# Performance work log

Measured on AMD Instinct MI355X. Metric: run time of the kernel, lower is better.

## Reference

```python
import jax, jax.numpy as jnp
import numpy as np

T, B, V, HID, L = 1024, 64, 256, 512, 2


def setup_inputs() -> dict:
    key = jax.random.key(0)
    ks = jax.random.split(key, 6)
    inputs = jax.random.normal(ks[0], (T, B, V), jnp.float32)
    H = jax.random.normal(ks[1], (L, B, HID), jnp.float32) * 0.1
    s1 = 1.0 / np.sqrt(V + HID)   # torch Linear default init bound
    W_net = jax.random.uniform(ks[2], (HID, V + HID), jnp.float32, -s1, s1)
    b_net = jax.random.uniform(ks[3], (HID,), jnp.float32, -s1, s1)
    s2 = 1.0 / np.sqrt(2 * HID)
    W_deep = jax.random.uniform(ks[4], (HID, 2 * HID), jnp.float32, -s2, s2)
    b_deep = jax.random.uniform(ks[5], (HID,), jnp.float32, -s2, s2)
    return {"inputs": inputs, "H": H, "W_net": W_net, "b_net": b_net,
            "W_deep": W_deep, "b_deep": b_deep}


def _rnn_scan(xs, h0, W, b):
    # xs: [T, B, Din], h0: [B, HID]; torch does tanh(cat(x, h) @ W.T + b)
    Din = xs.shape[-1]
    Wx, Wh = W[:, :Din], W[:, Din:]  # split cat-matmul into two GEMMs (same math)
    def step(h, x):
        h = jnp.tanh(x @ Wx.T + h @ Wh.T + b)
        return h, h
    last, states = jax.lax.scan(step, h0, xs)
    return states, last  # [T, B, HID], [B, HID]


def reference(inputs, H, W_net, b_net, W_deep, b_deep):
    all_states, last = _rnn_scan(inputs, H[0], W_net, b_net)
    last_states = [last]
    for l in range(1, H.shape[0]):  # deep layers: input dim = HID
        all_states, last = _rnn_scan(all_states, H[l], W_deep, b_deep)
        last_states.append(last)
    return all_states, jnp.stack(last_states)  # [T,B,HID], [L,B,HID]
```

## Files before the change

### kernel.cpp

```cpp
#include <hip/hip_runtime.h>
#include <hip/hip_fp16.h>
#include <cstdint>
#include <cstddef>

#define TT 1024
#define BB 64
#define VV 256
#define HH 512
static const size_t TBH = (size_t)TT * BB * HH;

#define AGENT __HIP_MEMORY_SCOPE_AGENT

typedef _Float16 half2v __attribute__((ext_vector_type(2)));
union U32H2 { unsigned u; half2v h; };

__device__ __forceinline__ unsigned pack_f16x2(float a, float b) {
    __half ha = __float2half_rn(a);
    __half hb = __float2half_rn(b);
    return (unsigned)__half_as_ushort(ha) | ((unsigned)__half_as_ushort(hb) << 16);
}

__device__ __forceinline__ float tanh_fast(float x) {
    float ax = fabsf(x);
    float e = __expf(-2.0f * ax);
    float r = (1.0f - e) * __builtin_amdgcn_rcpf(1.0f + e);
    return copysignf(r, x);
}

__device__ __forceinline__ float fdot2(unsigned w, unsigned h, float acc) {
    U32H2 uw; uw.u = w;
    U32H2 uh; uh.u = h;
#if __has_builtin(__builtin_amdgcn_fdot2)
    return __builtin_amdgcn_fdot2(uw.h, uh.h, acc, false);
#else
    return acc + (float)uw.h[0] * (float)uh.h[0] + (float)uw.h[1] * (float)uh.h[1];
#endif
}

__global__ void pack_weights(const float* __restrict__ Wnet,
                             const float* __restrict__ Wdeep,
                             unsigned* __restrict__ Wq0, unsigned* __restrict__ Wq1,
                             unsigned* __restrict__ Wp0, unsigned* __restrict__ Wp1) {
    int id = blockIdx.x * 256 + threadIdx.x;
    const int NQ  = HH * (HH / 2);
    const int NP0 = (VV / 2) * HH;
    const int NP1 = (HH / 2) * HH;
    if (id < NQ) {
        int i = id >> 8, jp = id & 255;
        const float* row = Wnet + (size_t)i * (VV + HH) + VV;
        Wq0[id] = pack_f16x2(row[2 * jp], row[2 * jp + 1]);
        return;
    }
    id -= NQ;
    if (id < NQ) {
        int i = id >> 8, jp = id & 255;
        const float* row = Wdeep + (size_t)i * (2 * HH) + HH;
        Wq1[id] = pack_f16x2(row[2 * jp], row[2 * jp + 1]);
        return;
    }
    id -= NQ;
    if (id < NP0) {
        int k2 = id >> 9, n = id & 511;
        const float* row = Wnet + (size_t)n * (VV + HH);
        Wp0[id] = pack_f16x2(row[2 * k2], row[2 * k2 + 1]);
        return;
    }
    id -= NP0;
    if (id < NP1) {
        int k2 = id >> 9, n = id & 511;
        const float* row = Wdeep + (size_t)n * (2 * HH);
        Wp1[id] = pack_f16x2(row[2 * k2], row[2 * k2 + 1]);
        return;
    }
}

__device__ __forceinline__ void dot8(float* acc, unsigned a, uint4 w0, uint4 w1) {
    acc[0] = fdot2(w0.x, a, acc[0]);
    acc[1] = fdot2(w0.y, a, acc[1]);
    acc[2] = fdot2(w0.z, a, acc[2]);
    acc[3] = fdot2(w0.w, a, acc[3]);
    acc[4] = fdot2(w1.x, a, acc[4]);
    acc[5] = fdot2(w1.y, a, acc[5]);
    acc[6] = fdot2(w1.z, a, acc[6]);
    acc[7] = fdot2(w1.w, a, acc[7]);
}

__launch_bounds__(1024)
__global__ void xproj_f16(const float* __restrict__ A,
                          const unsigned* __restrict__ Wp,
                          const float* __restrict__ bias,
                          float* __restrict__ C, int K) {
    extern __shared__ unsigned As2[];
    const int m0 = blockIdx.x * 32;
    const int t = threadIdx.x;
    const int K2 = K >> 1;

    const int nf4 = 8 * K;
    const float4* Ag = (const float4*)(A + (size_t)m0 * K);
    for (int idx = t; idx < nf4; idx += 1024) {
        float4 v = Ag[idx];
        As2[idx * 2]     = pack_f16x2(v.x, v.y);
        As2[idx * 2 + 1] = pack_f16x2(v.z, v.w);
    }
    __syncthreads();

    const int rg = t >> 6;
    const int n0 = (t & 63) * 8;

    float acc0[8] = {0, 0, 0, 0, 0, 0, 0, 0};
    float acc1[8] = {0, 0, 0, 0, 0, 0, 0, 0};

    const unsigned* a0p = As2 + (size_t)(rg * 2) * K2;
    const unsigned* a1p = a0p + K2;

#pragma unroll 4
    for (int k2 = 0; k2 < K2; k2 += 2) {
        unsigned a00 = a0p[k2], a01 = a0p[k2 + 1];
        unsigned a10 = a1p[k2], a11 = a1p[k2 + 1];
        const uint4 w00 = *(const uint4*)(Wp + (size_t)k2 * 512 + n0);
        const uint4 w01 = *(const uint4*)(Wp + (size_t)k2 * 512 + n0 + 4);
        const uint4 w10 = *(const uint4*)(Wp + (size_t)(k2 + 1) * 512 + n0);
        const uint4 w11 = *(const uint4*)(Wp + (size_t)(k2 + 1) * 512 + n0 + 4);
        dot8(acc0, a00, w00, w01);
        dot8(acc1, a10, w00, w01);
        dot8(acc0, a01, w10, w11);
        dot8(acc1, a11, w10, w11);
    }

    float bv[8];
#pragma unroll
    for (int c = 0; c < 8; ++c) bv[c] = bias[n0 + c];

    float* Crow0 = C + (size_t)(m0 + rg * 2) * 512 + n0;
    float* Crow1 = Crow0 + 512;
    *(float4*)(Crow0)     = make_float4(acc0[0] + bv[0], acc0[1] + bv[1], acc0[2] + bv[2], acc0[3] + bv[3]);
    *(float4*)(Crow0 + 4) = make_float4(acc0[4] + bv[4], acc0[5] + bv[5], acc0[6] + bv[6], acc0[7] + bv[7]);
    *(float4*)(Crow1)     = make_float4(acc1[0] + bv[0], acc1[1] + bv[1], acc1[2] + bv[2], acc1[3] + bv[3]);
    *(float4*)(Crow1 + 4) = make_float4(acc1[4] + bv[4], acc1[5] + bv[5], acc1[6] + bv[6], acc1[7] + bv[7]);
}

__launch_bounds__(512, 1)
__global__ void rnn_scan3(const unsigned* __restrict__ Wq,
                          const float* __restrict__ h0,
                          float* __restrict__ states,
                          float* __restrict__ last,
                          unsigned long long* __restrict__ X) {
    __shared__ float hsh[2][256];

    const int w = blockIdx.x;
    const int b = w & 63;
    const int s = w >> 6;
    const int r = threadIdx.x;
    const int lane = r & 63;
    const int owner = r >> 8;
    const bool is_owner = (owner == s);

    uint4 wreg[32];
    {
        const uint4* Wr = (const uint4*)(Wq + (size_t)r * 256 + s * 128);
#pragma unroll
        for (int q = 0; q < 32; ++q) wreg[q] = Wr[q];
    }

    unsigned hp[2];
    {
        const float2* h2 = (const float2*)(h0 + (size_t)b * HH);
#pragma unroll
        for (int rr = 0; rr < 2; ++rr) {
            float2 v = h2[s * 128 + rr * 64 + lane];
            hp[rr] = pack_f16x2(v.x, v.y);
        }
    }

    unsigned long long* slotA = X + ((((size_t)b * 2 + owner) * 2 + 0) << 8) + (r & 255);
    unsigned long long* slotB = slotA + 256;

    size_t base = (size_t)b * HH;
    const size_t tstride = (size_t)BB * HH;

    float pre_cur = 0.f;
    if (is_owner) pre_cur = states[base + r];

    float h = 0.f;
    for (int t = 0; t < TT; ++t) {
        float pre_nxt = 0.f;
        if (is_owner && t + 1 < TT) pre_nxt = states[base + tstride + r];

        float a0 = 0.f, a1 = 0.f, a2 = 0.f, a3 = 0.f;
#pragma unroll
        for (int q = 0; q < 32; ++q) {
            const uint4 wv = wreg[q];
            const int j = q * 4;
            unsigned s0 = (unsigned)__builtin_amdgcn_readlane((int)hp[(j + 0) >> 6], (j + 0) & 63);
            unsigned s1 = (unsigned)__builtin_amdgcn_readlane((int)hp[(j + 1) >> 6], (j + 1) & 63);
            unsigned s2 = (unsigned)__builtin_amdgcn_readlane((int)hp[(j + 2) >> 6], (j + 2) & 63);
            unsigned s3 = (unsigned)__builtin_amdgcn_readlane((int)hp[(j + 3) >> 6], (j + 3) & 63);
            a0 = fdot2(wv.x, s0, a0);
            a1 = fdot2(wv.y, s1, a1);
            a2 = fdot2(wv.z, s2, a2);
            a3 = fdot2(wv.w, s3, a3);
        }
        float part = (a0 + a1) + (a2 + a3);

        const int p = t & 1;
        unsigned long long* slot = p ? slotB : slotA;
        if (!is_owner) {
            unsigned long long msg = ((unsigned long long)(unsigned)(t + 1) << 32)
                                   | (unsigned long long)__float_as_uint(part);
            __hip_atomic_store(slot, msg, __ATOMIC_RELAXED, AGENT);
        } else {
            unsigned long long v;
            do {
                v = __hip_atomic_load(slot, __ATOMIC_RELAXED, AGENT);
            } while ((unsigned)(v >> 32) != (unsigned)(t + 1));
            float pother = __uint_as_float((unsigned)v);
            h = tanh_fast(pre_cur + part + pother);
            states[base + r] = h;
            hsh[p][r & 255] = h;
        }
        __syncthreads();

        const float2* hh = (const float2*)hsh[p];
#pragma unroll
        for (int rr = 0; rr < 2; ++rr) {
            float2 vv = hh[rr * 64 + lane];
            hp[rr] = pack_f16x2(vv.x, vv.y);
        }
        pre_cur = pre_nxt;
        base += tstride;
    }

    if (is_owner) last[(size_t)b * HH + r] = h;
}

extern "C" void kernel_launch(void* const* d_in, const int* in_sizes, int n_in,
                              void* d_out, int out_size, void* d_ws, size_t ws_size,
                              hipStream_t stream) {
    (void)in_sizes; (void)n_in; (void)out_size; (void)ws_size;
    const float* inputs = (const float*)d_in[0];
    const float* H      = (const float*)d_in[1];
    const float* Wnet   = (const float*)d_in[2];
    const float* bnet   = (const float*)d_in[3];
    const float* Wdeep  = (const float*)d_in[4];
    const float* bdeep  = (const float*)d_in[5];
    float* out = (float*)d_out;

    unsigned long long* X = (unsigned long long*)d_ws;
    unsigned* Wq0 = (unsigned*)(X + 64 * 2 * 2 * 256);
    unsigned* Wq1 = Wq0 + HH * (HH / 2);
    unsigned* Wp0 = Wq1 + HH * (HH / 2);
    unsigned* Wp1 = Wp0 + (VV / 2) * HH;

    hipLaunchKernelGGL(pack_weights, dim3(1792), dim3(256), 0, stream,
                       Wnet, Wdeep, Wq0, Wq1, Wp0, Wp1);

    hipLaunchKernelGGL(xproj_f16, dim3((TT * BB) / 32), dim3(1024),
                       32 * (VV / 2) * sizeof(unsigned), stream,
                       inputs, Wp0, bnet, out, VV);

    hipLaunchKernelGGL(rnn_scan3, dim3(128), dim3(512), 0, stream,
                       Wq0, H, out, out + TBH, X);

    hipLaunchKernelGGL(xproj_f16, dim3((TT * BB) / 32), dim3(1024),
                       32 * (HH / 2) * sizeof(unsigned), stream,
                       out, Wp1, bdeep, out, HH);

    hipLaunchKernelGGL(rnn_scan3, dim3(128), dim3(512), 0, stream,
                       Wq1, H + (size_t)BB * HH, out, out + TBH + (size_t)BB * HH, X);
}
```

Before: 4.054 ms.

## Run each batch's recurrence in one block and register-block the input projection

The recurrent scan now uses one 512-thread block per batch element instead of two cooperating blocks. This removes the per-step cross-block handshake through global atomics. Most of each thread's weight row sits in registers and the remaining slices sit in LDS, so each thread does twice the dot-product work per step. The hidden state is exchanged through a half-precision LDS buffer. Separately, the input-projection GEMM is rewritten to stage weight tiles in LDS and compute an 8-row by 8-column register tile per thread with 256-thread blocks.

```diff
diff --git a/kernel.cpp b/kernel.cpp
--- a/kernel.cpp
+++ b/kernel.cpp
@@ -8,8 +8,6 @@
 #define VV 256
 #define HH 512
 static const size_t TBH = (size_t)TT * BB * HH;
-
-#define AGENT __HIP_MEMORY_SCOPE_AGENT
 
 typedef _Float16 half2v __attribute__((ext_vector_type(2)));
 union U32H2 { unsigned u; half2v h; };
@@ -85,110 +83,128 @@
     acc[7] = fdot2(w1.w, a, acc[7]);
 }
 
-__launch_bounds__(1024)
+__launch_bounds__(256, 2)
 __global__ void xproj_f16(const float* __restrict__ A,
                           const unsigned* __restrict__ Wp,
                           const float* __restrict__ bias,
-                          float* __restrict__ C, int K) {
-    extern __shared__ unsigned As2[];
+                          float* __restrict__ C, int K2) {
+    extern __shared__ unsigned lds[];
+    unsigned* As2 = lds;
+    unsigned* Wt  = lds + 32 * K2;
     const int m0 = blockIdx.x * 32;
     const int t = threadIdx.x;
-    const int K2 = K >> 1;
-
-    const int nf4 = 8 * K;
-    const float4* Ag = (const float4*)(A + (size_t)m0 * K);
-    for (int idx = t; idx < nf4; idx += 1024) {
+
+    const int nf4 = 16 * K2;
+    const float4* Ag = (const float4*)(A + (size_t)m0 * (2 * K2));
+    for (int idx = t; idx < nf4; idx += 256) {
         float4 v = Ag[idx];
         As2[idx * 2]     = pack_f16x2(v.x, v.y);
         As2[idx * 2 + 1] = pack_f16x2(v.z, v.w);
     }
-    __syncthreads();
-
+
+    const int c  = t & 63;
     const int rg = t >> 6;
-    const int n0 = (t & 63) * 8;
-
-    float acc0[8] = {0, 0, 0, 0, 0, 0, 0, 0};
-    float acc1[8] = {0, 0, 0, 0, 0, 0, 0, 0};
-
-    const unsigned* a0p = As2 + (size_t)(rg * 2) * K2;
-    const unsigned* a1p = a0p + K2;
-
-#pragma unroll 4
-    for (int k2 = 0; k2 < K2; k2 += 2) {
-        unsigned a00 = a0p[k2], a01 = a0p[k2 + 1];
-        unsigned a10 = a1p[k2], a11 = a1p[k2 + 1];
-        const uint4 w00 = *(const uint4*)(Wp + (size_t)k2 * 512 + n0);
-        const uint4 w01 = *(const uint4*)(Wp + (size_t)k2 * 512 + n0 + 4);
-        const uint4 w10 = *(const uint4*)(Wp + (size_t)(k2 + 1) * 512 + n0);
-        const uint4 w11 = *(const uint4*)(Wp + (size_t)(k2 + 1) * 512 + n0 + 4);
-        dot8(acc0, a00, w00, w01);
-        dot8(acc1, a10, w00, w01);
-        dot8(acc0, a01, w10, w11);
-        dot8(acc1, a11, w10, w11);
+    const int n0 = c * 4;
+
+    float acc[8][8];
+#pragma unroll
+    for (int r = 0; r < 8; ++r)
+#pragma unroll
+        for (int j = 0; j < 8; ++j) acc[r][j] = 0.f;
+
+    for (int k0 = 0; k0 < K2; k0 += 16) {
+        __syncthreads();
+        {
+            const uint4* Wg = (const uint4*)(Wp + (size_t)k0 * 512);
+            uint4* Wt4 = (uint4*)Wt;
+#pragma unroll
+            for (int u = 0; u < 8; ++u) Wt4[t + u * 256] = Wg[t + u * 256];
+        }
+        __syncthreads();
+
+#pragma unroll
+        for (int kk = 0; kk < 16; kk += 2) {
+            uint4 wA0 = *(const uint4*)(Wt + kk * 512 + n0);
+            uint4 wB0 = *(const uint4*)(Wt + kk * 512 + n0 + 256);
+            uint4 wA1 = *(const uint4*)(Wt + (kk + 1) * 512 + n0);
+            uint4 wB1 = *(const uint4*)(Wt + (kk + 1) * 512 + n0 + 256);
+#pragma unroll
+            for (int r = 0; r < 8; ++r) {
+                uint2 a = *(const uint2*)(As2 + (size_t)(rg * 8 + r) * K2 + k0 + kk);
+                dot8(acc[r], a.x, wA0, wB0);
+                dot8(acc[r], a.y, wA1, wB1);
+            }
+        }
     }
 
     float bv[8];
 #pragma unroll
-    for (int c = 0; c < 8; ++c) bv[c] = bias[n0 + c];
-
-    float* Crow0 = C + (size_t)(m0 + rg * 2) * 512 + n0;
-    float* Crow1 = Crow0 + 512;
-    *(float4*)(Crow0)     = make_float4(acc0[0] + bv[0], acc0[1] + bv[1], acc0[2] + bv[2], acc0[3] + bv[3]);
-    *(float4*)(Crow0 + 4) = make_float4(acc0[4] + bv[4], acc0[5] + bv[5], acc0[6] + bv[6], acc0[7] + bv[7]);
-    *(float4*)(Crow1)     = make_float4(acc1[0] + bv[0], acc1[1] + bv[1], acc1[2] + bv[2], acc1[3] + bv[3]);
-    *(float4*)(Crow1 + 4) = make_float4(acc1[4] + bv[4], acc1[5] + bv[5], acc1[6] + bv[6], acc1[7] + bv[7]);
-}
-
-__launch_bounds__(512, 1)
-__global__ void rnn_scan3(const unsigned* __restrict__ Wq,
+    for (int j = 0; j < 4; ++j) { bv[j] = bias[n0 + j]; bv[4 + j] = bias[n0 + 256 + j]; }
+
+#pragma unroll
+    for (int r = 0; r < 8; ++r) {
+        float* Crow = C + (size_t)(m0 + rg * 8 + r) * 512;
+        *(float4*)(Crow + n0)       = make_float4(acc[r][0] + bv[0], acc[r][1] + bv[1],
+                                                  acc[r][2] + bv[2], acc[r][3] + bv[3]);
+        *(float4*)(Crow + n0 + 256) = make_float4(acc[r][4] + bv[4], acc[r][5] + bv[5],
+                                                  acc[r][6] + bv[6], acc[r][7] + bv[7]);
+    }
+}
+
+#define NVQ 57
+#define NLQ 7
+
+__launch_bounds__(512, 2)
+__global__ void rnn_scan4(const unsigned* __restrict__ Wq,
                           const float* __restrict__ h0,
                           float* __restrict__ states,
-                          float* __restrict__ last,
-                          unsigned long long* __restrict__ X) {
-    __shared__ float hsh[2][256];
-
-    const int w = blockIdx.x;
-    const int b = w & 63;
-    const int s = w >> 6;
+                          float* __restrict__ last) {
+    __shared__ uint4 Wlds[NLQ][HH];
+    __shared__ unsigned short hsh[2][HH];
+
+    const int b = blockIdx.x;
     const int r = threadIdx.x;
     const int lane = r & 63;
-    const int owner = r >> 8;
-    const bool is_owner = (owner == s);
-
-    uint4 wreg[32];
+
+    for (int idx = r; idx < NLQ * HH; idx += 512) {
+        int q = idx >> 9, row = idx & 511;
+        Wlds[q][row] = ((const uint4*)(Wq + (size_t)row * 256))[NVQ + q];
+    }
+
+    uint4 wreg[NVQ];
     {
-        const uint4* Wr = (const uint4*)(Wq + (size_t)r * 256 + s * 128);
-#pragma unroll
-        for (int q = 0; q < 32; ++q) wreg[q] = Wr[q];
-    }
-
-    unsigned hp[2];
+        const uint4* Wr = (const uint4*)(Wq + (size_t)r * 256);
+#pragma unroll
+        for (int q = 0; q < NVQ; ++q) {
+            uint4 v = Wr[q];
+            asm volatile("" : "+v"(v.x), "+v"(v.y), "+v"(v.z), "+v"(v.w));
+            wreg[q] = v;
+        }
+    }
+
+    unsigned hp[4];
     {
-        const float2* h2 = (const float2*)(h0 + (size_t)b * HH);
-#pragma unroll
-        for (int rr = 0; rr < 2; ++rr) {
-            float2 v = h2[s * 128 + rr * 64 + lane];
+        const float2* h02 = (const float2*)(h0 + (size_t)b * HH);
+#pragma unroll
+        for (int rr = 0; rr < 4; ++rr) {
+            float2 v = h02[rr * 64 + lane];
             hp[rr] = pack_f16x2(v.x, v.y);
         }
     }
-
-    unsigned long long* slotA = X + ((((size_t)b * 2 + owner) * 2 + 0) << 8) + (r & 255);
-    unsigned long long* slotB = slotA + 256;
-
-    size_t base = (size_t)b * HH;
+    __syncthreads();
+
     const size_t tstride = (size_t)BB * HH;
-
-    float pre_cur = 0.f;
-    if (is_owner) pre_cur = states[base + r];
-
+    const float* sp = states + (size_t)b * HH + r;
+    float* spw = states + (size_t)b * HH + r;
+    float pre_cur = *sp;
     float h = 0.f;
+
     for (int t = 0; t < TT; ++t) {
-        float pre_nxt = 0.f;
-        if (is_owner && t + 1 < TT) pre_nxt = states[base + tstride + r];
+        float pre_nxt = sp[tstride];
 
         float a0 = 0.f, a1 = 0.f, a2 = 0.f, a3 = 0.f;
 #pragma unroll
-        for (int q = 0; q < 32; ++q) {
+        for (int q = 0; q < NVQ; ++q) {
             const uint4 wv = wreg[q];
             const int j = q * 4;
             unsigned s0 = (unsigned)__builtin_amdgcn_readlane((int)hp[(j + 0) >> 6], (j + 0) & 63);
@@ -200,37 +216,37 @@
             a2 = fdot2(wv.z, s2, a2);
             a3 = fdot2(wv.w, s3, a3);
         }
+#pragma unroll
+        for (int q = 0; q < NLQ; ++q) {
+            const uint4 wv = Wlds[q][r];
+            const int j = (NVQ + q) * 4;
+            unsigned s0 = (unsigned)__builtin_amdgcn_readlane((int)hp[(j + 0) >> 6], (j + 0) & 63);
+            unsigned s1 = (unsigned)__builtin_amdgcn_readlane((int)hp[(j + 1) >> 6], (j + 1) & 63);
+            unsigned s2 = (unsigned)__builtin_amdgcn_readlane((int)hp[(j + 2) >> 6], (j + 2) & 63);
+            unsigned s3 = (unsigned)__builtin_amdgcn_readlane((int)hp[(j + 3) >> 6], (j + 3) & 63);
+            a0 = fdot2(wv.x, s0, a0);
+            a1 = fdot2(wv.y, s1, a1);
+            a2 = fdot2(wv.z, s2, a2);
+            a3 = fdot2(wv.w, s3, a3);
+        }
         float part = (a0 + a1) + (a2 + a3);
 
+        h = tanh_fast(pre_cur + part);
+        *spw = h;
+
         const int p = t & 1;
-        unsigned long long* slot = p ? slotB : slotA;
-        if (!is_owner) {
-            unsigned long long msg = ((unsigned long long)(unsigned)(t + 1) << 32)
-                                   | (unsigned long long)__float_as_uint(part);
-            __hip_atomic_store(slot, msg, __ATOMIC_RELAXED, AGENT);
-        } else {
-            unsigned long long v;
-            do {
-                v = __hip_atomic_load(slot, __ATOMIC_RELAXED, AGENT);
-            } while ((unsigned)(v >> 32) != (unsigned)(t + 1));
-            float pother = __uint_as_float((unsigned)v);
-            h = tanh_fast(pre_cur + part + pother);
-            states[base + r] = h;
-            hsh[p][r & 255] = h;
-        }
+        hsh[p][r] = (unsigned short)__half_as_ushort(__float2half_rn(h));
         __syncthreads();
-
-        const float2* hh = (const float2*)hsh[p];
-#pragma unroll
-        for (int rr = 0; rr < 2; ++rr) {
-            float2 vv = hh[rr * 64 + lane];
-            hp[rr] = pack_f16x2(vv.x, vv.y);
-        }
+        const unsigned* hh32 = (const unsigned*)&hsh[p][0];
+#pragma unroll
+        for (int rr = 0; rr < 4; ++rr) hp[rr] = hh32[rr * 64 + lane];
+
         pre_cur = pre_nxt;
-        base += tstride;
-    }
-
-    if (is_owner) last[(size_t)b * HH + r] = h;
+        sp  += tstride;
+        spw += tstride;
+    }
+
+    last[(size_t)b * HH + r] = h;
 }
 
 extern "C" void kernel_launch(void* const* d_in, const int* in_sizes, int n_in,
@@ -245,8 +261,7 @@
     const float* bdeep  = (const float*)d_in[5];
     float* out = (float*)d_out;
 
-    unsigned long long* X = (unsigned long long*)d_ws;
-    unsigned* Wq0 = (unsigned*)(X + 64 * 2 * 2 * 256);
+    unsigned* Wq0 = (unsigned*)d_ws;
     unsigned* Wq1 = Wq0 + HH * (HH / 2);
     unsigned* Wp0 = Wq1 + HH * (HH / 2);
     unsigned* Wp1 = Wp0 + (VV / 2) * HH;
@@ -254,17 +269,17 @@
     hipLaunchKernelGGL(pack_weights, dim3(1792), dim3(256), 0, stream,
                        Wnet, Wdeep, Wq0, Wq1, Wp0, Wp1);
 
-    hipLaunchKernelGGL(xproj_f16, dim3((TT * BB) / 32), dim3(1024),
-                       32 * (VV / 2) * sizeof(unsigned), stream,
-                       inputs, Wp0, bnet, out, VV);
-
-    hipLaunchKernelGGL(rnn_scan3, dim3(128), dim3(512), 0, stream,
-                       Wq0, H, out, out + TBH, X);
-
-    hipLaunchKernelGGL(xproj_f16, dim3((TT * BB) / 32), dim3(1024),
-                       32 * (HH / 2) * sizeof(unsigned), stream,
-                       out, Wp1, bdeep, out, HH);
-
-    hipLaunchKernelGGL(rnn_scan3, dim3(128), dim3(512), 0, stream,
-                       Wq1, H + (size_t)BB * HH, out, out + TBH + (size_t)BB * HH, X);
-}
+    hipLaunchKernelGGL(xproj_f16, dim3((TT * BB) / 32), dim3(256),
+                       (32 * (VV / 2) + 16 * 512) * sizeof(unsigned), stream,
+                       inputs, Wp0, bnet, out, VV / 2);
+
+    hipLaunchKernelGGL(rnn_scan4, dim3(BB), dim3(512), 0, stream,
+                       Wq0, H, out, out + TBH);
+
+    hipLaunchKernelGGL(xproj_f16, dim3((TT * BB) / 32), dim3(256),
+                       (32 * (HH / 2) + 16 * 512) * sizeof(unsigned), stream,
+                       out, Wp1, bdeep, out, HH / 2);
+
+    hipLaunchKernelGGL(rnn_scan4, dim3(BB), dim3(512), 0, stream,
+                       Wq1, H + (size_t)BB * HH, out, out + TBH + (size_t)BB * HH);
+}
```

Result: slower. 5.021 ms (+23.9%).
